# Optimization experiments

Measured on AMD Instinct MI355X. Metric: run time of the kernel, lower is better.

The kernel has to match this reference:

```python
import jax, jax.numpy as jnp
import numpy as np

B, T, C, H = 2, 2048, 1024, 16
HS = C // H        # head dim = 64
HALF = HS // 2     # rope half = 32


def _rope_cos_sin():
    # standard RoPE frequencies over the half-dim
    inv_freq = 1.0 / (10000.0 ** (np.arange(HALF, dtype=np.float32) / HALF))
    t = np.arange(T, dtype=np.float32)
    ang = np.outer(t, inv_freq)  # [T, HALF]
    cos = np.cos(ang)[None, None]  # [1,1,T,HALF]
    sin = np.sin(ang)[None, None]
    return jnp.asarray(cos), jnp.asarray(sin)


def setup_inputs() -> dict:
    key = jax.random.key(0)
    k1, k2, k3 = jax.random.split(key, 3)
    cos, sin = _rope_cos_sin()
    return {
        "x": jax.random.normal(k1, (B, T, C), dtype=jnp.float32),
        "cos": cos,
        "sin": sin,
        "w_attn": jax.random.normal(k2, (C, 3 * C), dtype=jnp.float32) * (1.0 / np.sqrt(C)),
        "b_attn": jnp.zeros((3 * C,), dtype=jnp.float32),
        "w_proj": jax.random.normal(k3, (C, C), dtype=jnp.float32) * (1.0 / np.sqrt(C)),
        "b_proj": jnp.zeros((C,), dtype=jnp.float32),
    }


def _rope_apply(x, cos, sin):
    # x: [B,H,T,HS]; cos/sin: [1,1,T,HALF]
    x1, x2 = x[..., :HALF], x[..., HALF:]
    return jnp.concatenate([x1 * cos - x2 * sin, x1 * sin + x2 * cos], axis=-1)


def reference(x, cos, sin, w_attn, b_attn, w_proj, b_proj):
    b, t, c = x.shape
    qkv = x @ w_attn + b_attn                      # [B,T,3C]
    q, k, v = jnp.split(qkv, 3, axis=-1)
    # [B,T,C] -> [B,H,T,HS]
    def to_heads(u):
        return u.reshape(b, t, H, HS).transpose(0, 2, 1, 3)
    q, k, v = to_heads(q), to_heads(k), to_heads(v)
    q = _rope_apply(q, cos[:, :, :t], sin[:, :, :t])
    k = _rope_apply(k, cos[:, :, :t], sin[:, :, :t])
    scale = 1.0 / np.sqrt(HS).astype(np.float32)
    scores = jnp.einsum("bhqd,bhkd->bhqk", q, k) * scale
    causal = jnp.tril(jnp.ones((t, t), dtype=bool))
    scores = jnp.where(causal, scores, jnp.finfo(scores.dtype).min)
    attn = jax.nn.softmax(scores, axis=-1)
    ctx = jnp.einsum("bhqk,bhkd->bhqd", attn, v)   # [B,H,T,HS]
    ctx = ctx.transpose(0, 2, 1, 3).reshape(b, t, c)
    return ctx @ w_proj + b_proj
```

## Files before the change

### kernel.cpp

```cpp
#include <hip/hip_runtime.h>
#include <hip/hip_bf16.h>

#define Bn    2
#define Tdim  2048
#define Cdim  1024
#define Hn    16
#define HSd   64
#define Mrows 4096

typedef unsigned short u16;
typedef __attribute__((ext_vector_type(8))) short short8;
typedef __attribute__((ext_vector_type(4))) float f32x4;

__device__ __forceinline__ u16 f2bf(float f) {
  union { __hip_bfloat16 h; u16 u; } cv;
  cv.h = __float2bfloat16(f);
  return cv.u;
}

#define GLOAD_LDS16(g, l)                                                     \
  __builtin_amdgcn_global_load_lds(                                           \
      (const __attribute__((address_space(1))) void*)(g),                     \
      (__attribute__((address_space(3))) void*)(l), 16, 0, 0)

#define CFENCE asm volatile("" ::: "memory")

__global__ __launch_bounds__(256) void k_prep(const float* __restrict__ x,
                                              u16* __restrict__ xb,
                                              const float* __restrict__ wattn,
                                              u16* __restrict__ wattnT,
                                              const float* __restrict__ wproj,
                                              u16* __restrict__ wprojT) {
  __shared__ float tile[64][65];
  const int bid = blockIdx.x, tid = threadIdx.x;
  if (bid < 4096) {
    int i = bid * 256 + tid;
    float4 v = ((const float4*)x)[i];
    unsigned o0 = (unsigned)f2bf(v.x) | ((unsigned)f2bf(v.y) << 16);
    unsigned o1 = (unsigned)f2bf(v.z) | ((unsigned)f2bf(v.w) << 16);
    ((uint2*)xb)[i] = make_uint2(o0, o1);
    return;
  }
  const float* in;
  u16* out;
  int Cc, c0, r0;
  if (bid < 4096 + 768) {
    int b = bid - 4096;
    in = wattn; out = wattnT; Cc = 3072;
    c0 = (b % 48) * 64; r0 = (b / 48) * 64;
  } else {
    int b = bid - 4864;
    in = wproj; out = wprojT; Cc = 1024;
    c0 = (b % 16) * 64; r0 = (b / 16) * 64;
  }
  const int R = 1024;
  int lc = tid & 63, l0 = tid >> 6;
  for (int rr = l0; rr < 64; rr += 4)
    tile[rr][lc] = in[(size_t)(r0 + rr) * Cc + c0 + lc];
  __syncthreads();
  for (int rr = l0; rr < 64; rr += 4)
    out[(size_t)(c0 + rr) * R + r0 + lc] = f2bf(tile[lc][rr]);
}

__global__ __launch_bounds__(256) void k_transpose_v(const u16* __restrict__ Vh,
                                                     u16* __restrict__ Vt) {
  __shared__ u16 tile[64][72];
  int bh = blockIdx.y, t0 = blockIdx.x * 64;
  int lc = threadIdx.x & 63, l0 = threadIdx.x >> 6;
  const u16* src = Vh + (size_t)bh * Tdim * HSd;
  u16* dst = Vt + (size_t)bh * HSd * Tdim;
  for (int rr = l0; rr < 64; rr += 4)
    tile[rr][lc] = src[(size_t)(t0 + rr) * HSd + lc];
  __syncthreads();
  for (int dd = l0; dd < 64; dd += 4)
    dst[(size_t)dd * Tdim + t0 + lc] = tile[lc][dd];
}

template <int EPI, int BM, int BN, int WM, int WN, int MINW>
__global__ __launch_bounds__(64 * WM * WN, MINW) void k_gemm2(
    const u16* __restrict__ A, const u16* __restrict__ Bt,
    const float* __restrict__ bias, const float* __restrict__ cosT,
    const float* __restrict__ sinT, u16* __restrict__ Qh, u16* __restrict__ Kh,
    u16* __restrict__ Vh, float* __restrict__ Out, int Ndim, int Kdim) {
  __shared__ u16 As[2][BM * 32];
  __shared__ u16 Bs[2][BN * 32];
  const int tid = threadIdx.x;
  const int wid = tid >> 6, lane = tid & 63;
  const int wr = wid / WN, wc = wid % WN;
  const int lr = lane & 15, lg = lane >> 4;
  const int m0 = blockIdx.x * BM, n0 = blockIdx.y * BN;
  const int wm = wr * 64, wn = wc * 64;

  f32x4 acc[4][4] = {};

  const u16* Ag = A + (size_t)m0 * Kdim;
  const u16* Bg = Bt + (size_t)n0 * Kdim;
  const int srw = lane >> 2;
  const int scb = ((lane & 3) ^ ((lane >> 3) & 3)) << 4;
  constexpr int NW = WM * WN;
  constexpr int CPW = (BM + BN) / 16 / NW;
  constexpr int CA = BM / 16;

#define STAGE2(bi, t)                                                         \
  do {                                                                        \
    _Pragma("unroll") for (int cc = 0; cc < CPW; ++cc) {                      \
      int c = wid * CPW + cc;                                                 \
      if (c < CA)                                                             \
        GLOAD_LDS16(                                                          \
            (const char*)(Ag + (size_t)(c * 16 + srw) * Kdim + (t)*32) + scb, \
            As[bi] + c * 512);                                                \
      else                                                                    \
        GLOAD_LDS16((const char*)(Bg + (size_t)((c - CA) * 16 + srw) * Kdim + \
                                  (t)*32) +                                   \
                        scb,                                                  \
                    Bs[bi] + (c - CA) * 512);                                 \
    }                                                                         \
  } while (0)

#define LDFRAG(buf, row)                                                      \
  (*(const short8*)((const char*)(buf) + (row)*64 +                           \
                    ((lg * 16) ^ ((((row) >> 1) & 3) << 4))))

  const int nt = Kdim >> 5;
  STAGE2(0, 0);
  asm volatile("s_waitcnt vmcnt(0)" ::: "memory");
  __builtin_amdgcn_s_barrier();
  CFENCE;

  int cur = 0;
  for (int t = 0; t < nt; ++t) {
    if (t + 1 < nt) STAGE2(cur ^ 1, t + 1);
    const u16* ab = As[cur];
    const u16* bb = Bs[cur];
    short8 a[4], b[4];
#pragma unroll
    for (int i = 0; i < 4; ++i) a[i] = LDFRAG(ab, wm + i * 16 + lr);
#pragma unroll
    for (int j = 0; j < 4; ++j) b[j] = LDFRAG(bb, wn + j * 16 + lr);
    asm volatile("s_waitcnt lgkmcnt(0)" ::: "memory");
    __builtin_amdgcn_sched_barrier(0);
    __builtin_amdgcn_s_setprio(1);
#pragma unroll
    for (int i = 0; i < 4; ++i)
#pragma unroll
      for (int j = 0; j < 4; ++j)
        acc[i][j] =
            __builtin_amdgcn_mfma_f32_16x16x32_bf16(a[i], b[j], acc[i][j], 0, 0, 0);
    __builtin_amdgcn_s_setprio(0);
    CFENCE;
    asm volatile("s_waitcnt vmcnt(0)" ::: "memory");
    __builtin_amdgcn_s_barrier();
    CFENCE;
    cur ^= 1;
  }
#undef STAGE2
#undef LDFRAG

  const int nbase = n0 + wn;
  if (EPI == 0) {
    const int sec = nbase >> 10;
    const int hh = (nbase & 1023) >> 6;
    const float qs = (sec == 0) ? 0.125f : 1.0f;
    float bj[4];
#pragma unroll
    for (int nj = 0; nj < 4; ++nj) bj[nj] = bias[nbase + nj * 16 + lr];
#pragma unroll
    for (int mi = 0; mi < 4; ++mi) {
      int growb = m0 + wm + mi * 16 + 4 * lg;
#pragma unroll
      for (int r = 0; r < 4; ++r) {
        int gr = growb + r;
        int bI = gr >> 11, tq = gr & (Tdim - 1);
        size_t off = ((size_t)(bI * Hn + hh) * Tdim + tq) * HSd;
        if (sec < 2) {
          u16* dst = (sec == 0) ? Qh : Kh;
#pragma unroll
          for (int nj = 0; nj < 2; ++nj) {
            int d = nj * 16 + lr;
            float v1 = acc[mi][nj][r] + bj[nj];
            float v2 = acc[mi][nj + 2][r] + bj[nj + 2];
            float cs = cosT[tq * 32 + d], sn = sinT[tq * 32 + d];
            dst[off + d] = f2bf((v1 * cs - v2 * sn) * qs);
            dst[off + d + 32] = f2bf((v1 * sn + v2 * cs) * qs);
          }
        } else {
#pragma unroll
          for (int nj = 0; nj < 4; ++nj)
            Vh[off + nj * 16 + lr] = f2bf(acc[mi][nj][r] + bj[nj]);
        }
      }
    }
  } else {
#pragma unroll
    for (int mi = 0; mi < 4; ++mi) {
      int growb = m0 + wm + mi * 16 + 4 * lg;
#pragma unroll
      for (int r = 0; r < 4; ++r) {
        int gr = growb + r;
#pragma unroll
        for (int nj = 0; nj < 4; ++nj) {
          int col = nbase + nj * 16 + lr;
          Out[(size_t)gr * Ndim + col] = acc[mi][nj][r] + bias[col];
        }
      }
    }
  }
}

__global__ __launch_bounds__(512, 4) void k_attn(const u16* __restrict__ Qh,
                                                 const u16* __restrict__ Kh,
                                                 const u16* __restrict__ Vt,
                                                 u16* __restrict__ ctx) {
  __shared__ u16 Ks[2][64 * 64];
  __shared__ u16 Vs[2][64 * 64];
  __shared__ u16 Plds[8][16][72];
  const int tid = threadIdx.x;
  const int wid = tid >> 6, lane = tid & 63;
  const int lr = lane & 15, lg = lane >> 4;
  const int bid = blockIdx.x;
  const int xb = 15 - (bid >> 5);
  const int bh = bid & 31;
  const int qr0 = xb * 128 + wid * 16;
  const int nt = 2 * xb + 2;
  const int itd = qr0 >> 6;
  const u16* Q = Qh + (size_t)bh * Tdim * HSd;
  const u16* K = Kh + (size_t)bh * Tdim * HSd;
  const u16* V = Vt + (size_t)bh * HSd * Tdim;

  short8 qf0 = *(const short8*)(Q + (size_t)(qr0 + lr) * HSd + 8 * lg);
  short8 qf1 = *(const short8*)(Q + (size_t)(qr0 + lr) * HSd + 32 + 8 * lg);

  const int srow = lane >> 3;
  const int scol = 16 * ((lane & 7) ^ srow);
  const int swz = (lr & 7) << 4;

  f32x4 ctxa[4] = {};
  float ssum[4] = {0.f, 0.f, 0.f, 0.f};
  const float L2E = 1.44269504089f;
  const float MC = 24.0f * L2E;
  const f32x4 zero = {};

#define STAGE_KV(b, kv0)                                                      \
  do {                                                                        \
    GLOAD_LDS16((const char*)(K + (size_t)((kv0) + wid * 8 + srow) * HSd) +   \
                    scol,                                                     \
                Ks[b] + wid * 8 * 64);                                        \
    GLOAD_LDS16((const char*)(V + (size_t)(wid * 8 + srow) * Tdim + (kv0)) +  \
                    scol,                                                     \
                Vs[b] + wid * 8 * 64);                                        \
  } while (0)

  STAGE_KV(0, 0);
  __syncthreads();

  int cur = 0;
  for (int it = 0; it < nt; ++it) {
    const int kv0 = it * 64;
    if (it + 1 < nt) STAGE_KV(cur ^ 1, kv0 + 64);

    if (it <= itd) {
      const char* ksb = (const char*)(Ks[cur]);
      const char* vsb = (const char*)(Vs[cur]);

      f32x4 s[4];
#pragma unroll
      for (int f = 0; f < 4; ++f) {
        int row = 16 * f + lr;
        int c0 = (lg * 16) ^ swz;
        short8 kf0 = *(const short8*)(ksb + row * 128 + c0);
        short8 kf1 = *(const short8*)(ksb + row * 128 + (c0 ^ 64));
        s[f] = __builtin_amdgcn_mfma_f32_16x16x32_bf16(qf0, kf0, zero, 0, 0, 0);
        s[f] = __builtin_amdgcn_mfma_f32_16x16x32_bf16(qf1, kf1, s[f], 0, 0, 0);
      }

#pragma unroll
      for (int r = 0; r < 4; ++r) {
        if (it == itd) {
          int q = qr0 + 4 * lg + r;
#pragma unroll
          for (int f = 0; f < 4; ++f)
            if (kv0 + 16 * f + lr > q) s[f][r] = -1e30f;
        }
#pragma unroll
        for (int f = 0; f < 4; ++f) {
          float p = __builtin_amdgcn_exp2f(fmaf(s[f][r], L2E, -MC));
          ssum[r] += p;
          Plds[wid][4 * lg + r][16 * f + lr] = f2bf(p);
        }
      }

      const char* pb = (const char*)(&Plds[wid][0][0]);
      short8 pa0 = *(const short8*)(pb + lr * 144 + lg * 16);
      short8 pa1 = *(const short8*)(pb + lr * 144 + 64 + lg * 16);

#pragma unroll
      for (int dt = 0; dt < 4; ++dt) {
        int row = 16 * dt + lr;
        int c0 = (lg * 16) ^ swz;
        short8 vb0 = *(const short8*)(vsb + row * 128 + c0);
        short8 vb1 = *(const short8*)(vsb + row * 128 + (c0 ^ 64));
        ctxa[dt] =
            __builtin_amdgcn_mfma_f32_16x16x32_bf16(pa0, vb0, ctxa[dt], 0, 0, 0);
        ctxa[dt] =
            __builtin_amdgcn_mfma_f32_16x16x32_bf16(pa1, vb1, ctxa[dt], 0, 0, 0);
      }
    }

    __syncthreads();
    cur ^= 1;
  }
#undef STAGE_KV

  const int bI = bh >> 4, hh = bh & 15;
#pragma unroll
  for (int r = 0; r < 4; ++r) {
    float s = ssum[r];
    s += __shfl_xor(s, 1);
    s += __shfl_xor(s, 2);
    s += __shfl_xor(s, 4);
    s += __shfl_xor(s, 8);
    float inv = 1.0f / s;
    int t = qr0 + 4 * lg + r;
    size_t off = ((size_t)bI * Tdim + t) * Cdim + hh * HSd;
#pragma unroll
    for (int dt = 0; dt < 4; dt++)
      ctx[off + dt * 16 + lr] = f2bf(ctxa[dt][r] * inv);
  }
}

extern "C" void kernel_launch(void* const* d_in, const int* in_sizes, int n_in,
                              void* d_out, int out_size, void* d_ws,
                              size_t ws_size, hipStream_t stream) {
  const float* x = (const float*)d_in[0];
  const float* cosT = (const float*)d_in[1];
  const float* sinT = (const float*)d_in[2];
  const float* wattn = (const float*)d_in[3];
  const float* battn = (const float*)d_in[4];
  const float* wproj = (const float*)d_in[5];
  const float* bproj = (const float*)d_in[6];
  float* out = (float*)d_out;
  char* ws = (char*)d_ws;
  const size_t MB = 1024 * 1024;
  u16* xb = (u16*)(ws + 0);
  u16* Vt = (u16*)(ws + 0);
  u16* wattnT = (u16*)(ws + 8 * MB);
  u16* wprojT = (u16*)(ws + 14 * MB);
  u16* Qh = (u16*)(ws + 16 * MB);
  u16* Kh = (u16*)(ws + 24 * MB);
  u16* Vh = (u16*)(ws + 32 * MB);
  u16* ctx = (u16*)(ws + 40 * MB);

  k_prep<<<5120, 256, 0, stream>>>(x, xb, wattn, wattnT, wproj, wprojT);
  k_gemm2<0, 128, 128, 2, 2, 4><<<dim3(32, 24), 256, 0, stream>>>(
      xb, wattnT, battn, cosT, sinT, Qh, Kh, Vh, nullptr, 3072, 1024);
  k_transpose_v<<<dim3(32, 32), 256, 0, stream>>>(Vh, Vt);
  k_attn<<<512, 512, 0, stream>>>(Qh, Kh, Vt, ctx);
  k_gemm2<1, 128, 64, 2, 1, 4><<<dim3(32, 16), 128, 0, stream>>>(
      ctx, wprojT, bproj, nullptr, nullptr, nullptr, nullptr, nullptr, out,
      1024, 1024);
}
```

Before: 209.6 us.

## Fuse V transpose into QKV GEMM epilogue and compute softmax row sums via MFMA

Removes the separate V transpose kernel by staging each warp's V tile in shared memory with an XOR swizzle inside the QKV GEMM epilogue and writing it out directly in transposed layout. In attention, the softmax denominator is now accumulated with an extra MFMA against a ones vector instead of per-lane adds plus a cross-lane shuffle reduction. P is converted to bf16 with a cheaper bit-rounding routine. This saves one kernel launch and a round trip of V through global memory. In exchange the V epilogue issues 64 narrow strided global stores per lane, the softmax sum is taken over the bf16-rounded P values, and the staging buffer reuses the GEMM's A tile shared memory.

```diff
diff --git a/kernel.cpp b/kernel.cpp
--- a/kernel.cpp
+++ b/kernel.cpp
@@ -16,6 +16,9 @@
   union { __hip_bfloat16 h; u16 u; } cv;
   cv.h = __float2bfloat16(f);
   return cv.u;
+}
+__device__ __forceinline__ u16 f2bf_fast(float f) {
+  return (u16)((__float_as_uint(f) + 0x8000u) >> 16);
 }
 
 #define GLOAD_LDS16(g, l)                                                     \
@@ -62,26 +65,12 @@
     out[(size_t)(c0 + rr) * R + r0 + lc] = f2bf(tile[lc][rr]);
 }
 
-__global__ __launch_bounds__(256) void k_transpose_v(const u16* __restrict__ Vh,
-                                                     u16* __restrict__ Vt) {
-  __shared__ u16 tile[64][72];
-  int bh = blockIdx.y, t0 = blockIdx.x * 64;
-  int lc = threadIdx.x & 63, l0 = threadIdx.x >> 6;
-  const u16* src = Vh + (size_t)bh * Tdim * HSd;
-  u16* dst = Vt + (size_t)bh * HSd * Tdim;
-  for (int rr = l0; rr < 64; rr += 4)
-    tile[rr][lc] = src[(size_t)(t0 + rr) * HSd + lc];
-  __syncthreads();
-  for (int dd = l0; dd < 64; dd += 4)
-    dst[(size_t)dd * Tdim + t0 + lc] = tile[lc][dd];
-}
-
 template <int EPI, int BM, int BN, int WM, int WN, int MINW>
 __global__ __launch_bounds__(64 * WM * WN, MINW) void k_gemm2(
     const u16* __restrict__ A, const u16* __restrict__ Bt,
     const float* __restrict__ bias, const float* __restrict__ cosT,
     const float* __restrict__ sinT, u16* __restrict__ Qh, u16* __restrict__ Kh,
-    u16* __restrict__ Vh, float* __restrict__ Out, int Ndim, int Kdim) {
+    u16* __restrict__ Vt, float* __restrict__ Out, int Ndim, int Kdim) {
   __shared__ u16 As[2][BM * 32];
   __shared__ u16 Bs[2][BN * 32];
   const int tid = threadIdx.x;
@@ -160,20 +149,20 @@
   if (EPI == 0) {
     const int sec = nbase >> 10;
     const int hh = (nbase & 1023) >> 6;
-    const float qs = (sec == 0) ? 0.125f : 1.0f;
     float bj[4];
 #pragma unroll
     for (int nj = 0; nj < 4; ++nj) bj[nj] = bias[nbase + nj * 16 + lr];
-#pragma unroll
-    for (int mi = 0; mi < 4; ++mi) {
-      int growb = m0 + wm + mi * 16 + 4 * lg;
-#pragma unroll
-      for (int r = 0; r < 4; ++r) {
-        int gr = growb + r;
-        int bI = gr >> 11, tq = gr & (Tdim - 1);
-        size_t off = ((size_t)(bI * Hn + hh) * Tdim + tq) * HSd;
-        if (sec < 2) {
-          u16* dst = (sec == 0) ? Qh : Kh;
+    if (sec < 2) {
+      const float qs = (sec == 0) ? 0.125f : 1.0f;
+      u16* dst = (sec == 0) ? Qh : Kh;
+#pragma unroll
+      for (int mi = 0; mi < 4; ++mi) {
+        int growb = m0 + wm + mi * 16 + 4 * lg;
+#pragma unroll
+        for (int r = 0; r < 4; ++r) {
+          int gr = growb + r;
+          int bI = gr >> 11, tq = gr & (Tdim - 1);
+          size_t off = ((size_t)(bI * Hn + hh) * Tdim + tq) * HSd;
 #pragma unroll
           for (int nj = 0; nj < 2; ++nj) {
             int d = nj * 16 + lr;
@@ -183,11 +172,30 @@
             dst[off + d] = f2bf((v1 * cs - v2 * sn) * qs);
             dst[off + d + 32] = f2bf((v1 * sn + v2 * cs) * qs);
           }
-        } else {
-#pragma unroll
-          for (int nj = 0; nj < 4; ++nj)
-            Vh[off + nj * 16 + lr] = f2bf(acc[mi][nj][r] + bj[nj]);
-        }
+        }
+      }
+    } else {
+      __builtin_amdgcn_s_barrier();
+      u16* vt = (u16*)(&As[0][0]) + wid * 4096;
+#pragma unroll
+      for (int mi = 0; mi < 4; ++mi)
+#pragma unroll
+        for (int r = 0; r < 4; ++r) {
+          int tl = mi * 16 + 4 * lg + r;
+#pragma unroll
+          for (int nj = 0; nj < 4; ++nj) {
+            int d = nj * 16 + lr;
+            vt[tl * 64 + (d ^ tl)] = f2bf(acc[mi][nj][r] + bj[nj]);
+          }
+        }
+      asm volatile("s_waitcnt lgkmcnt(0)" ::: "memory");
+      int gr0 = m0 + wm;
+      int bI = gr0 >> 11, t0 = gr0 & (Tdim - 1);
+      u16* dst = Vt + (size_t)(bI * Hn + hh) * HSd * Tdim;
+#pragma unroll 8
+      for (int dd = 0; dd < 64; ++dd) {
+        u16 val = vt[lane * 64 + (dd ^ lane)];
+        dst[(size_t)dd * Tdim + t0 + lane] = val;
       }
     }
   } else {
@@ -235,7 +243,9 @@
   const int swz = (lr & 7) << 4;
 
   f32x4 ctxa[4] = {};
-  float ssum[4] = {0.f, 0.f, 0.f, 0.f};
+  f32x4 sacc = {};
+  const short8 ones = {0x3F80, 0x3F80, 0x3F80, 0x3F80,
+                       0x3F80, 0x3F80, 0x3F80, 0x3F80};
   const float L2E = 1.44269504089f;
   const float MC = 24.0f * L2E;
   const f32x4 zero = {};
@@ -284,14 +294,16 @@
 #pragma unroll
         for (int f = 0; f < 4; ++f) {
           float p = __builtin_amdgcn_exp2f(fmaf(s[f][r], L2E, -MC));
-          ssum[r] += p;
-          Plds[wid][4 * lg + r][16 * f + lr] = f2bf(p);
+          Plds[wid][4 * lg + r][16 * f + lr] = f2bf_fast(p);
         }
       }
 
       const char* pb = (const char*)(&Plds[wid][0][0]);
       short8 pa0 = *(const short8*)(pb + lr * 144 + lg * 16);
       short8 pa1 = *(const short8*)(pb + lr * 144 + 64 + lg * 16);
+
+      sacc = __builtin_amdgcn_mfma_f32_16x16x32_bf16(pa0, ones, sacc, 0, 0, 0);
+      sacc = __builtin_amdgcn_mfma_f32_16x16x32_bf16(pa1, ones, sacc, 0, 0, 0);
 
 #pragma unroll
       for (int dt = 0; dt < 4; ++dt) {
@@ -314,12 +326,7 @@
   const int bI = bh >> 4, hh = bh & 15;
 #pragma unroll
   for (int r = 0; r < 4; ++r) {
-    float s = ssum[r];
-    s += __shfl_xor(s, 1);
-    s += __shfl_xor(s, 2);
-    s += __shfl_xor(s, 4);
-    s += __shfl_xor(s, 8);
-    float inv = 1.0f / s;
+    float inv = 1.0f / sacc[r];
     int t = qr0 + 4 * lg + r;
     size_t off = ((size_t)bI * Tdim + t) * Cdim + hh * HSd;
 #pragma unroll
@@ -342,18 +349,16 @@
   char* ws = (char*)d_ws;
   const size_t MB = 1024 * 1024;
   u16* xb = (u16*)(ws + 0);
-  u16* Vt = (u16*)(ws + 0);
   u16* wattnT = (u16*)(ws + 8 * MB);
   u16* wprojT = (u16*)(ws + 14 * MB);
   u16* Qh = (u16*)(ws + 16 * MB);
   u16* Kh = (u16*)(ws + 24 * MB);
-  u16* Vh = (u16*)(ws + 32 * MB);
+  u16* Vt = (u16*)(ws + 32 * MB);
   u16* ctx = (u16*)(ws + 40 * MB);
 
   k_prep<<<5120, 256, 0, stream>>>(x, xb, wattn, wattnT, wproj, wprojT);
   k_gemm2<0, 128, 128, 2, 2, 4><<<dim3(32, 24), 256, 0, stream>>>(
-      xb, wattnT, battn, cosT, sinT, Qh, Kh, Vh, nullptr, 3072, 1024);
-  k_transpose_v<<<dim3(32, 32), 256, 0, stream>>>(Vh, Vt);
+      xb, wattnT, battn, cosT, sinT, Qh, Kh, Vt, nullptr, 3072, 1024);
   k_attn<<<512, 512, 0, stream>>>(Qh, Kh, Vt, ctx);
   k_gemm2<1, 128, 64, 2, 1, 4><<<dim3(32, 16), 128, 0, stream>>>(
       ctx, wprojT, bproj, nullptr, nullptr, nullptr, nullptr, nullptr, out,
```

New measurement: 196.8 us. -6.1%, faster.
